# Kernel optimization log

Hardware: AMD Instinct MI355X
Metric: run time of the kernel (lower is better)

The kernel has to match this reference:

```python
import jax, jax.numpy as jnp
import numpy as np

N_NODES = 100000
N_REL = 3
HID = 256
LN_EPS = 1e-5
DENOM_EPS = 1e-8


def setup_inputs() -> dict:
    key = jax.random.key(0)
    ks = jax.random.split(key, 8)
    E = 300000
    return {
        "feat_text": jax.random.normal(ks[0], (N_NODES, 384), dtype=jnp.float32),
        "feat_image": jax.random.normal(ks[1], (N_NODES, 512), dtype=jnp.float32),
        "W_text": jax.random.normal(ks[2], (384, HID), dtype=jnp.float32) * 0.05,
        "W_image": jax.random.normal(ks[3], (512, HID), dtype=jnp.float32) * 0.05,
        "W_rel": jax.random.normal(ks[4], (N_REL, HID, HID), dtype=jnp.float32) * 0.05,
        "ln_gamma": jnp.ones((HID,), dtype=jnp.float32),
        "ln_beta": jnp.zeros((HID,), dtype=jnp.float32),
        "edge_weight": jax.random.uniform(ks[5], (E,), dtype=jnp.float32),
        "edge_index": jax.random.randint(ks[6], (2, E), 0, N_NODES),
        "edge_type": jax.random.randint(ks[7], (E,), 0, N_REL),
    }


def _layer_norm(x, gamma, beta):
    mu = jnp.mean(x, axis=-1, keepdims=True)
    var = jnp.mean(jnp.square(x - mu), axis=-1, keepdims=True)
    return (x - mu) * jax.lax.rsqrt(var + LN_EPS) * gamma + beta


def reference(feat_text, feat_image, W_text, W_image, W_rel, ln_gamma, ln_beta,
              edge_weight, edge_index, edge_type):
    # base embedding: mean of per-modality projections (fuse_mode='avg'), node 0 zeroed
    h0 = 0.5 * (feat_text @ W_text + feat_image @ W_image)  # [N, H]
    h0 = h0.at[0].set(0.0)

    src = edge_index[0]
    dst = edge_index[1]
    h_src = h0[src]  # [E, H] gather once, reused per relation

    aggregated = jnp.zeros_like(h0)
    for rel in range(N_REL):  # small fixed relation count
        w = jnp.where(edge_type == rel, edge_weight, 0.0)          # [E]
        msgs = (h_src @ W_rel[rel]) * w[:, None]                    # [E, H]
        agg_rel = jax.ops.segment_sum(msgs, dst, num_segments=N_NODES)   # [N, H]
        denom = jax.ops.segment_sum(w, dst, num_segments=N_NODES)        # [N]
        aggregated = aggregated + agg_rel / jnp.maximum(denom, DENOM_EPS)[:, None]

    # dropout=0.0 (identity)
    h1 = _layer_norm(h0 + aggregated, ln_gamma, ln_beta)
    h1 = h1.at[0].set(0.0)
    return h1
```

## Files before the change

kernel.cpp:

```cpp
#include <hip/hip_runtime.h>
#include <hip/hip_bf16.h>

#define HID 256
#define LN_EPS 1e-5f
#define DENOM_EPS 1e-8f

typedef __attribute__((ext_vector_type(8))) short short8;
typedef __attribute__((ext_vector_type(4))) float f32x4;

#define WP1_ELEMS (28 * 256 * 32)
#define WP2_ELEMS (24 * 256 * 32)

__device__ inline unsigned bfpk(float x, float y) {
    __hip_bfloat162 h = __float22bfloat162_rn(make_float2(x, y));
    return *reinterpret_cast<unsigned*>(&h);
}

__device__ inline void gld16(const void* g, void* l) {
    __builtin_amdgcn_global_load_lds(
        (const __attribute__((address_space(1))) void*)g,
        (__attribute__((address_space(3))) void*)l, 16, 0, 0);
}

__global__ __launch_bounds__(256) void kpack(
    const float* __restrict__ wt, const float* __restrict__ wi,
    const float* __restrict__ wrel,
    __hip_bfloat16* __restrict__ wp1, __hip_bfloat16* __restrict__ wp2)
{
    int idx = blockIdx.x * 256 + threadIdx.x;
    if (idx < WP1_ELEMS) {
        int kk = idx & 31, col = (idx >> 5) & 255, ks = idx >> 13;
        int k = ks * 32 + kk;
        float v = (k < 384) ? wt[k * 256 + col] : wi[(k - 384) * 256 + col];
        wp1[idx] = __float2bfloat16(v * 0.5f);
    } else {
        int j = idx - WP1_ELEMS;
        if (j < WP2_ELEMS) {
            int kk = j & 31, col = (j >> 5) & 255, ks = j >> 13;
            int k = ks * 32 + kk;
            wp2[j] = __float2bfloat16(wrel[k * 256 + col]);
        }
    }
}

__global__ __launch_bounds__(256) void kchain(
    const int* __restrict__ edst, int* __restrict__ head, int* __restrict__ nxt, int E)
{
    int e = blockIdx.x * 256 + threadIdx.x;
    if (e < E) nxt[e] = atomicExch(&head[edst[e]], e);
}

__global__ __launch_bounds__(256) void k2_gather(
    const float* __restrict__ h0, const int* __restrict__ esrc,
    const int* __restrict__ etype, const float* __restrict__ ew,
    const int* __restrict__ head, const int* __restrict__ nxt,
    __hip_bfloat16* __restrict__ S, int N)
{
    int gid = blockIdx.x * 256 + threadIdx.x;
    int d = gid >> 6;
    int lane = gid & 63;
    if (d >= N) return;

    f32x4 a0 = {0.f, 0.f, 0.f, 0.f}, a1 = a0, a2 = a0;
    float d0 = 0.f, d1 = 0.f, d2 = 0.f;

    int e = head[d];
    while (e >= 0) {
        int src = esrc[e];
        int ty = etype[e];
        float w = ew[e];
        const float4 h = *(const float4*)(h0 + (size_t)src * HID + lane * 4);
        f32x4 hw = {w * h.x, w * h.y, w * h.z, w * h.w};
        if (ty == 0)      { a0 += hw; d0 += w; }
        else if (ty == 1) { a1 += hw; d1 += w; }
        else              { a2 += hw; d2 += w; }
        e = nxt[e];
    }

    float i0 = 1.0f / fmaxf(d0, DENOM_EPS);
    float i1 = 1.0f / fmaxf(d1, DENOM_EPS);
    float i2 = 1.0f / fmaxf(d2, DENOM_EPS);
    __hip_bfloat16* row = S + (size_t)d * 768;
    uint2 p;
    p = make_uint2(bfpk(a0[0] * i0, a0[1] * i0), bfpk(a0[2] * i0, a0[3] * i0));
    *(uint2*)(row + 0   + lane * 4) = p;
    p = make_uint2(bfpk(a1[0] * i1, a1[1] * i1), bfpk(a1[2] * i1, a1[3] * i1));
    *(uint2*)(row + 256 + lane * 4) = p;
    p = make_uint2(bfpk(a2[0] * i2, a2[1] * i2), bfpk(a2[2] * i2, a2[3] * i2));
    *(uint2*)(row + 512 + lane * 4) = p;
}

template<int MODE>
__global__ __launch_bounds__(256, 4) void kgemm(
    const float* __restrict__ a0, const float* __restrict__ a1,
    const __hip_bfloat16* __restrict__ Sb,
    const __hip_bfloat16* __restrict__ wp,
    const float* h0in, const float* __restrict__ gamma,
    const float* __restrict__ beta, float* out, int N)
{
    constexpr int NSTEPS = MODE ? 24 : 28;
    constexpr int TB = MODE ? 4096 : 8192;
    __shared__ __align__(16) unsigned char As[3][TB];
    __shared__ float redS[MODE ? 64 : 1][4];
    __shared__ float redQ[MODE ? 64 : 1][4];

    const int t = threadIdx.x;
    const int lane = t & 63;
    const int w = t >> 6;
    const int m0 = blockIdx.x * 64;
    const int g = lane >> 4;

    auto stageA = [&](int ks, int buf) {
        if constexpr (MODE == 0) {
#pragma unroll
            for (int j = 0; j < 2; ++j) {
                int slot = j * 4 + w;
                int r = slot * 8 + (lane >> 3);
                int grow = m0 + r; if (grow >= N) grow = m0;
                int q = (lane & 7) ^ (lane >> 3);
                const float* src = (ks < 12)
                    ? (a0 + (size_t)grow * 384 + ks * 32 + q * 4)
                    : (a1 + (size_t)grow * 512 + (ks - 12) * 32 + q * 4);
                gld16(src, As[buf] + slot * 1024);
            }
        } else {
            int r = w * 16 + (lane >> 2);
            int grow = m0 + r; if (grow >= N) grow = m0;
            int q = (lane & 3) ^ ((lane >> 3) & 3);
            const __hip_bfloat16* src = Sb + (size_t)grow * 768 + ks * 32 + q * 8;
            gld16(src, As[buf] + w * 1024);
        }
    };

    f32x4 acc[4][4];
#pragma unroll
    for (int i = 0; i < 4; ++i)
#pragma unroll
        for (int j = 0; j < 4; ++j) acc[i][j] = (f32x4){0.f, 0.f, 0.f, 0.f};

    stageA(0, 0);

    for (int ks = 0; ks < NSTEPS; ++ks) {
        if (ks + 1 < NSTEPS) stageA(ks + 1, (ks + 1) % 3);
        short8 bf[4];
#pragma unroll
        for (int fc = 0; fc < 4; ++fc)
            bf[fc] = *(const short8*)((const short*)wp +
                      (size_t)(ks * 256 + w * 64 + fc * 16 + (lane & 15)) * 32 + g * 8);

        __syncthreads();

        const unsigned char* Ab = As[ks % 3];
        short8 af[4];
#pragma unroll
        for (int fr = 0; fr < 4; ++fr) {
            int r = fr * 16 + (lane & 15);
            if constexpr (MODE == 0) {
                const unsigned char* base = Ab + r * 128;
                f32x4 lo = *(const f32x4*)(base + ((2 * g) ^ (r & 7)) * 16);
                f32x4 hi = *(const f32x4*)(base + ((2 * g + 1) ^ (r & 7)) * 16);
                union { short8 s; unsigned u[4]; } cv;
                cv.u[0] = bfpk(lo[0], lo[1]);
                cv.u[1] = bfpk(lo[2], lo[3]);
                cv.u[2] = bfpk(hi[0], hi[1]);
                cv.u[3] = bfpk(hi[2], hi[3]);
                af[fr] = cv.s;
            } else {
                af[fr] = *(const short8*)(Ab + r * 64 + (g ^ ((r >> 1) & 3)) * 16);
            }
        }
#pragma unroll
        for (int fr = 0; fr < 4; ++fr)
#pragma unroll
            for (int fc = 0; fc < 4; ++fc)
                acc[fr][fc] = __builtin_amdgcn_mfma_f32_16x16x32_bf16(af[fr], bf[fc], acc[fr][fc], 0, 0, 0);
    }

    const int cbase = w * 64;

    if constexpr (MODE == 0) {
#pragma unroll
        for (int fr = 0; fr < 4; ++fr)
#pragma unroll
            for (int reg = 0; reg < 4; ++reg) {
                int grow = m0 + fr * 16 + g * 4 + reg;
                if (grow >= N) continue;
#pragma unroll
                for (int fc = 0; fc < 4; ++fc) {
                    float vv = acc[fr][fc][reg];
                    if (grow == 0) vv = 0.f;
                    out[(size_t)grow * 256 + cbase + fc * 16 + (lane & 15)] = vv;
                }
            }
    } else {
#pragma unroll
        for (int fr = 0; fr < 4; ++fr)
#pragma unroll
            for (int reg = 0; reg < 4; ++reg) {
                int grow = m0 + fr * 16 + g * 4 + reg;
                if (grow < N) {
#pragma unroll
                    for (int fc = 0; fc < 4; ++fc)
                        acc[fr][fc][reg] += h0in[(size_t)grow * 256 + cbase + fc * 16 + (lane & 15)];
                }
            }
#pragma unroll
        for (int fr = 0; fr < 4; ++fr)
#pragma unroll
            for (int reg = 0; reg < 4; ++reg) {
                float s = 0.f, q = 0.f;
#pragma unroll
                for (int fc = 0; fc < 4; ++fc) {
                    float vv = acc[fr][fc][reg];
                    s += vv; q += vv * vv;
                }
#pragma unroll
                for (int off = 1; off < 16; off <<= 1) {
                    s += __shfl_xor(s, off, 64);
                    q += __shfl_xor(q, off, 64);
                }
                if ((lane & 15) == 0) {
                    int rl = fr * 16 + g * 4 + reg;
                    redS[rl][w] = s;
                    redQ[rl][w] = q;
                }
            }
        __syncthreads();
        float g4[4], b4[4];
#pragma unroll
        for (int fc = 0; fc < 4; ++fc) {
            g4[fc] = gamma[cbase + fc * 16 + (lane & 15)];
            b4[fc] = beta[cbase + fc * 16 + (lane & 15)];
        }
#pragma unroll
        for (int fr = 0; fr < 4; ++fr)
#pragma unroll
            for (int reg = 0; reg < 4; ++reg) {
                int rl = fr * 16 + g * 4 + reg;
                int grow = m0 + rl;
                if (grow >= N) continue;
                float s = redS[rl][0] + redS[rl][1] + redS[rl][2] + redS[rl][3];
                float q = redQ[rl][0] + redQ[rl][1] + redQ[rl][2] + redQ[rl][3];
                float mu  = s * (1.f / 256.f);
                float var = q * (1.f / 256.f) - mu * mu;
                float rstd = rsqrtf(var + LN_EPS);
#pragma unroll
                for (int fc = 0; fc < 4; ++fc) {
                    float vv = (acc[fr][fc][reg] - mu) * rstd * g4[fc] + b4[fc];
                    if (grow == 0) vv = 0.f;
                    out[(size_t)grow * 256 + cbase + fc * 16 + (lane & 15)] = vv;
                }
            }
    }
}

extern "C" void kernel_launch(void* const* d_in, const int* in_sizes, int n_in,
                              void* d_out, int out_size, void* d_ws, size_t ws_size,
                              hipStream_t stream) {
    const int N = in_sizes[0] / 384;
    const int E = in_sizes[7];
    const float* ft    = (const float*)d_in[0];
    const float* fi    = (const float*)d_in[1];
    const float* wt    = (const float*)d_in[2];
    const float* wi    = (const float*)d_in[3];
    const float* wrel  = (const float*)d_in[4];
    const float* gamma = (const float*)d_in[5];
    const float* beta  = (const float*)d_in[6];
    const float* ew    = (const float*)d_in[7];
    const int*   eidx  = (const int*)d_in[8];
    const int*   etype = (const int*)d_in[9];
    float* out = (float*)d_out;

    __hip_bfloat16* S = (__hip_bfloat16*)d_ws;
    int* head = (int*)((char*)d_ws + (size_t)N * 768 * 2);
    int* nxt  = head + N;
    __hip_bfloat16* wp1 = (__hip_bfloat16*)(nxt + E);
    __hip_bfloat16* wp2 = wp1 + WP1_ELEMS;

    hipMemsetAsync(head, 0xFF, (size_t)N * sizeof(int), stream);

    kpack<<<(WP1_ELEMS + WP2_ELEMS + 255) / 256, 256, 0, stream>>>(wt, wi, wrel, wp1, wp2);

    kchain<<<(E + 255) / 256, 256, 0, stream>>>(eidx + E, head, nxt, E);

    const int gblocks = (N + 63) / 64;
    kgemm<0><<<gblocks, 256, 0, stream>>>(ft, fi, nullptr, wp1, nullptr, nullptr, nullptr, out, N);

    const int wblocks = (N + 3) / 4;
    k2_gather<<<wblocks, 256, 0, stream>>>(out, eidx, etype, ew, head, nxt, S, N);

    kgemm<1><<<gblocks, 256, 0, stream>>>(nullptr, nullptr, S, wp2, out, gamma, beta, out, N);
}
```

Before: 337.7 us.

## Drop LDS staging in GEMMs; gather writes MFMA-fragment layout for direct loads

The gather kernel now writes the aggregated relation features in a pre-tiled, MFMA-fragment-ordered layout per 64-row block, so the second GEMM can load A fragments straight from global memory without LDS staging or barriers. The first GEMM is split into its own kernel that reads fp32 features directly from global with per-lane vector loads and converts them to bf16 in registers. Gather blocks grow to 512 threads (8 nodes per block). This removes LDS traffic and syncs, but gives up async prefetch and multi-buffering, so more global-load latency is exposed, and the direct fp32 loads in the first GEMM may be less coalesced.

```diff
diff --git a/kernel.cpp b/kernel.cpp
--- a/kernel.cpp
+++ b/kernel.cpp
@@ -14,12 +14,6 @@
 __device__ inline unsigned bfpk(float x, float y) {
     __hip_bfloat162 h = __float22bfloat162_rn(make_float2(x, y));
     return *reinterpret_cast<unsigned*>(&h);
-}
-
-__device__ inline void gld16(const void* g, void* l) {
-    __builtin_amdgcn_global_load_lds(
-        (const __attribute__((address_space(1))) void*)g,
-        (__attribute__((address_space(3))) void*)l, 16, 0, 0);
 }
 
 __global__ __launch_bounds__(256) void kpack(
@@ -50,15 +44,15 @@
     if (e < E) nxt[e] = atomicExch(&head[edst[e]], e);
 }
 
-__global__ __launch_bounds__(256) void k2_gather(
+__global__ __launch_bounds__(512) void k2_gather(
     const float* __restrict__ h0, const int* __restrict__ esrc,
     const int* __restrict__ etype, const float* __restrict__ ew,
     const int* __restrict__ head, const int* __restrict__ nxt,
-    __hip_bfloat16* __restrict__ S, int N)
-{
-    int gid = blockIdx.x * 256 + threadIdx.x;
-    int d = gid >> 6;
-    int lane = gid & 63;
+    __hip_bfloat16* __restrict__ Sf, int N)
+{
+    int w = threadIdx.x >> 6;
+    int lane = threadIdx.x & 63;
+    int d = blockIdx.x * 8 + w;
     if (d >= N) return;
 
     f32x4 a0 = {0.f, 0.f, 0.f, 0.f}, a1 = a0, a2 = a0;
@@ -68,69 +62,45 @@
     while (e >= 0) {
         int src = esrc[e];
         int ty = etype[e];
-        float w = ew[e];
+        float w_ = ew[e];
         const float4 h = *(const float4*)(h0 + (size_t)src * HID + lane * 4);
-        f32x4 hw = {w * h.x, w * h.y, w * h.z, w * h.w};
-        if (ty == 0)      { a0 += hw; d0 += w; }
-        else if (ty == 1) { a1 += hw; d1 += w; }
-        else              { a2 += hw; d2 += w; }
+        f32x4 hw = {w_ * h.x, w_ * h.y, w_ * h.z, w_ * h.w};
+        if (ty == 0)      { a0 += hw; d0 += w_; }
+        else if (ty == 1) { a1 += hw; d1 += w_; }
+        else              { a2 += hw; d2 += w_; }
         e = nxt[e];
     }
 
     float i0 = 1.0f / fmaxf(d0, DENOM_EPS);
     float i1 = 1.0f / fmaxf(d1, DENOM_EPS);
     float i2 = 1.0f / fmaxf(d2, DENOM_EPS);
-    __hip_bfloat16* row = S + (size_t)d * 768;
-    uint2 p;
-    p = make_uint2(bfpk(a0[0] * i0, a0[1] * i0), bfpk(a0[2] * i0, a0[3] * i0));
-    *(uint2*)(row + 0   + lane * 4) = p;
-    p = make_uint2(bfpk(a1[0] * i1, a1[1] * i1), bfpk(a1[2] * i1, a1[3] * i1));
-    *(uint2*)(row + 256 + lane * 4) = p;
-    p = make_uint2(bfpk(a2[0] * i2, a2[1] * i2), bfpk(a2[2] * i2, a2[3] * i2));
-    *(uint2*)(row + 512 + lane * 4) = p;
-}
-
-template<int MODE>
-__global__ __launch_bounds__(256, 4) void kgemm(
-    const float* __restrict__ a0, const float* __restrict__ a1,
-    const __hip_bfloat16* __restrict__ Sb,
+
+    const int rb = d >> 6, r = d & 63;
+    const int g = (lane & 7) >> 1;
+    const int e0 = (lane & 1) * 4;
+    __hip_bfloat16* base = Sf + (size_t)rb * (24 * 256 * 8);
+#pragma unroll
+    for (int rel = 0; rel < 3; ++rel) {
+        const f32x4& a = rel == 0 ? a0 : (rel == 1 ? a1 : a2);
+        const float iv = rel == 0 ? i0 : (rel == 1 ? i1 : i2);
+        int ks = rel * 8 + (lane >> 3);
+        size_t off = ((size_t)ks * 256 + g * 64 + r) * 8 + e0;
+        uint2 p = make_uint2(bfpk(a[0] * iv, a[1] * iv), bfpk(a[2] * iv, a[3] * iv));
+        *(uint2*)(base + off) = p;
+    }
+}
+
+__global__ __launch_bounds__(256, 3) void kg0(
+    const float* __restrict__ ft, const float* __restrict__ fi,
     const __hip_bfloat16* __restrict__ wp,
-    const float* h0in, const float* __restrict__ gamma,
-    const float* __restrict__ beta, float* out, int N)
-{
-    constexpr int NSTEPS = MODE ? 24 : 28;
-    constexpr int TB = MODE ? 4096 : 8192;
-    __shared__ __align__(16) unsigned char As[3][TB];
-    __shared__ float redS[MODE ? 64 : 1][4];
-    __shared__ float redQ[MODE ? 64 : 1][4];
-
+    float* __restrict__ out, int N)
+{
     const int t = threadIdx.x;
     const int lane = t & 63;
     const int w = t >> 6;
     const int m0 = blockIdx.x * 64;
     const int g = lane >> 4;
-
-    auto stageA = [&](int ks, int buf) {
-        if constexpr (MODE == 0) {
-#pragma unroll
-            for (int j = 0; j < 2; ++j) {
-                int slot = j * 4 + w;
-                int r = slot * 8 + (lane >> 3);
-                int grow = m0 + r; if (grow >= N) grow = m0;
-                int q = (lane & 7) ^ (lane >> 3);
-                const float* src = (ks < 12)
-                    ? (a0 + (size_t)grow * 384 + ks * 32 + q * 4)
-                    : (a1 + (size_t)grow * 512 + (ks - 12) * 32 + q * 4);
-                gld16(src, As[buf] + slot * 1024);
-            }
-        } else {
-            int r = w * 16 + (lane >> 2);
-            int grow = m0 + r; if (grow >= N) grow = m0;
-            int q = (lane & 3) ^ ((lane >> 3) & 3);
-            const __hip_bfloat16* src = Sb + (size_t)grow * 768 + ks * 32 + q * 8;
-            gld16(src, As[buf] + w * 1024);
-        }
-    };
+    const int rl = lane & 15;
 
     f32x4 acc[4][4];
 #pragma unroll
@@ -138,37 +108,103 @@
 #pragma unroll
         for (int j = 0; j < 4; ++j) acc[i][j] = (f32x4){0.f, 0.f, 0.f, 0.f};
 
-    stageA(0, 0);
-
-    for (int ks = 0; ks < NSTEPS; ++ks) {
-        if (ks + 1 < NSTEPS) stageA(ks + 1, (ks + 1) % 3);
-        short8 bf[4];
-#pragma unroll
-        for (int fc = 0; fc < 4; ++fc)
-            bf[fc] = *(const short8*)((const short*)wp +
-                      (size_t)(ks * 256 + w * 64 + fc * 16 + (lane & 15)) * 32 + g * 8);
-
-        __syncthreads();
-
-        const unsigned char* Ab = As[ks % 3];
-        short8 af[4];
+    const short* wpb = (const short*)wp + ((size_t)w * 64 + rl) * 32 + g * 8;
+
+#pragma unroll 1
+    for (int seg = 0; seg < 2; ++seg) {
+        const float* __restrict__ A = seg ? fi : ft;
+        const int K = seg ? 512 : 384;
+        const int ns = seg ? 16 : 12;
+        const int ksb = seg ? 12 : 0;
+        const float* rp[4];
 #pragma unroll
         for (int fr = 0; fr < 4; ++fr) {
-            int r = fr * 16 + (lane & 15);
-            if constexpr (MODE == 0) {
-                const unsigned char* base = Ab + r * 128;
-                f32x4 lo = *(const f32x4*)(base + ((2 * g) ^ (r & 7)) * 16);
-                f32x4 hi = *(const f32x4*)(base + ((2 * g + 1) ^ (r & 7)) * 16);
-                union { short8 s; unsigned u[4]; } cv;
+            int grow = m0 + fr * 16 + rl;
+            if (grow >= N) grow = m0;
+            rp[fr] = A + (size_t)grow * K + g * 8;
+        }
+#pragma unroll 1
+        for (int s = 0; s < ns; ++s) {
+            short8 af[4];
+#pragma unroll
+            for (int fr = 0; fr < 4; ++fr) {
+                const float* ap = rp[fr] + s * 32;
+                f32x4 lo = *(const f32x4*)ap;
+                f32x4 hi = *(const f32x4*)(ap + 4);
+                union { short8 s8; unsigned u[4]; } cv;
                 cv.u[0] = bfpk(lo[0], lo[1]);
                 cv.u[1] = bfpk(lo[2], lo[3]);
                 cv.u[2] = bfpk(hi[0], hi[1]);
                 cv.u[3] = bfpk(hi[2], hi[3]);
-                af[fr] = cv.s;
-            } else {
-                af[fr] = *(const short8*)(Ab + r * 64 + (g ^ ((r >> 1) & 3)) * 16);
-            }
-        }
+                af[fr] = cv.s8;
+            }
+            short8 bf[4];
+            const short* bp = wpb + (size_t)(ksb + s) * 256 * 32;
+#pragma unroll
+            for (int fc = 0; fc < 4; ++fc)
+                bf[fc] = *(const short8*)(bp + fc * 16 * 32);
+#pragma unroll
+            for (int fr = 0; fr < 4; ++fr)
+#pragma unroll
+                for (int fc = 0; fc < 4; ++fc)
+                    acc[fr][fc] = __builtin_amdgcn_mfma_f32_16x16x32_bf16(af[fr], bf[fc], acc[fr][fc], 0, 0, 0);
+        }
+    }
+
+    const int cbase = w * 64;
+#pragma unroll
+    for (int fr = 0; fr < 4; ++fr)
+#pragma unroll
+        for (int reg = 0; reg < 4; ++reg) {
+            int grow = m0 + fr * 16 + g * 4 + reg;
+            if (grow >= N) continue;
+#pragma unroll
+            for (int fc = 0; fc < 4; ++fc) {
+                float vv = acc[fr][fc][reg];
+                if (grow == 0) vv = 0.f;
+                out[(size_t)grow * 256 + cbase + fc * 16 + rl] = vv;
+            }
+        }
+}
+
+__global__ __launch_bounds__(256, 4) void kg1(
+    const __hip_bfloat16* __restrict__ Sf,
+    const __hip_bfloat16* __restrict__ wp,
+    const float* h0in, const float* __restrict__ gamma,
+    const float* __restrict__ beta, float* __restrict__ out, int N)
+{
+    __shared__ float redS[64][4];
+    __shared__ float redQ[64][4];
+
+    const int t = threadIdx.x;
+    const int lane = t & 63;
+    const int w = t >> 6;
+    const int rb = blockIdx.x;
+    const int m0 = rb * 64;
+    const int g = lane >> 4;
+    const int rl = lane & 15;
+
+    f32x4 acc[4][4];
+#pragma unroll
+    for (int i = 0; i < 4; ++i)
+#pragma unroll
+        for (int j = 0; j < 4; ++j) acc[i][j] = (f32x4){0.f, 0.f, 0.f, 0.f};
+
+    const short* Ab = (const short*)(Sf + (size_t)rb * (24 * 256 * 8)) + ((size_t)g * 64 + rl) * 8;
+    const short* wpb = (const short*)wp + ((size_t)w * 64 + rl) * 32 + g * 8;
+
+#pragma unroll 1
+    for (int ks = 0; ks < 24; ++ks) {
+        short8 af[4];
+        const short* ap = Ab + (size_t)ks * 256 * 8;
+#pragma unroll
+        for (int fr = 0; fr < 4; ++fr)
+            af[fr] = *(const short8*)(ap + fr * 16 * 8);
+        short8 bf[4];
+        const short* bp = wpb + (size_t)ks * 256 * 32;
+#pragma unroll
+        for (int fc = 0; fc < 4; ++fc)
+            bf[fc] = *(const short8*)(bp + fc * 16 * 32);
 #pragma unroll
         for (int fr = 0; fr < 4; ++fr)
 #pragma unroll
@@ -177,81 +213,64 @@
     }
 
     const int cbase = w * 64;
-
-    if constexpr (MODE == 0) {
-#pragma unroll
-        for (int fr = 0; fr < 4; ++fr)
-#pragma unroll
-            for (int reg = 0; reg < 4; ++reg) {
-                int grow = m0 + fr * 16 + g * 4 + reg;
-                if (grow >= N) continue;
-#pragma unroll
-                for (int fc = 0; fc < 4; ++fc) {
-                    float vv = acc[fr][fc][reg];
-                    if (grow == 0) vv = 0.f;
-                    out[(size_t)grow * 256 + cbase + fc * 16 + (lane & 15)] = vv;
-                }
-            }
-    } else {
-#pragma unroll
-        for (int fr = 0; fr < 4; ++fr)
-#pragma unroll
-            for (int reg = 0; reg < 4; ++reg) {
-                int grow = m0 + fr * 16 + g * 4 + reg;
-                if (grow < N) {
-#pragma unroll
-                    for (int fc = 0; fc < 4; ++fc)
-                        acc[fr][fc][reg] += h0in[(size_t)grow * 256 + cbase + fc * 16 + (lane & 15)];
-                }
-            }
-#pragma unroll
-        for (int fr = 0; fr < 4; ++fr)
-#pragma unroll
-            for (int reg = 0; reg < 4; ++reg) {
-                float s = 0.f, q = 0.f;
-#pragma unroll
-                for (int fc = 0; fc < 4; ++fc) {
-                    float vv = acc[fr][fc][reg];
-                    s += vv; q += vv * vv;
-                }
-#pragma unroll
-                for (int off = 1; off < 16; off <<= 1) {
-                    s += __shfl_xor(s, off, 64);
-                    q += __shfl_xor(q, off, 64);
-                }
-                if ((lane & 15) == 0) {
-                    int rl = fr * 16 + g * 4 + reg;
-                    redS[rl][w] = s;
-                    redQ[rl][w] = q;
-                }
-            }
-        __syncthreads();
-        float g4[4], b4[4];
-#pragma unroll
-        for (int fc = 0; fc < 4; ++fc) {
-            g4[fc] = gamma[cbase + fc * 16 + (lane & 15)];
-            b4[fc] = beta[cbase + fc * 16 + (lane & 15)];
-        }
-#pragma unroll
-        for (int fr = 0; fr < 4; ++fr)
-#pragma unroll
-            for (int reg = 0; reg < 4; ++reg) {
-                int rl = fr * 16 + g * 4 + reg;
-                int grow = m0 + rl;
-                if (grow >= N) continue;
-                float s = redS[rl][0] + redS[rl][1] + redS[rl][2] + redS[rl][3];
-                float q = redQ[rl][0] + redQ[rl][1] + redQ[rl][2] + redQ[rl][3];
-                float mu  = s * (1.f / 256.f);
-                float var = q * (1.f / 256.f) - mu * mu;
-                float rstd = rsqrtf(var + LN_EPS);
-#pragma unroll
-                for (int fc = 0; fc < 4; ++fc) {
-                    float vv = (acc[fr][fc][reg] - mu) * rstd * g4[fc] + b4[fc];
-                    if (grow == 0) vv = 0.f;
-                    out[(size_t)grow * 256 + cbase + fc * 16 + (lane & 15)] = vv;
-                }
-            }
-    }
+#pragma unroll
+    for (int fr = 0; fr < 4; ++fr)
+#pragma unroll
+        for (int reg = 0; reg < 4; ++reg) {
+            int grow = m0 + fr * 16 + g * 4 + reg;
+            if (grow < N) {
+#pragma unroll
+                for (int fc = 0; fc < 4; ++fc)
+                    acc[fr][fc][reg] += h0in[(size_t)grow * 256 + cbase + fc * 16 + rl];
+            }
+        }
+#pragma unroll
+    for (int fr = 0; fr < 4; ++fr)
+#pragma unroll
+        for (int reg = 0; reg < 4; ++reg) {
+            float s = 0.f, q = 0.f;
+#pragma unroll
+            for (int fc = 0; fc < 4; ++fc) {
+                float vv = acc[fr][fc][reg];
+                s += vv; q += vv * vv;
+            }
+#pragma unroll
+            for (int off = 1; off < 16; off <<= 1) {
+                s += __shfl_xor(s, off, 64);
+                q += __shfl_xor(q, off, 64);
+            }
+            if (rl == 0) {
+                int rlidx = fr * 16 + g * 4 + reg;
+                redS[rlidx][w] = s;
+                redQ[rlidx][w] = q;
+            }
+        }
+    __syncthreads();
+    float g4[4], b4[4];
+#pragma unroll
+    for (int fc = 0; fc < 4; ++fc) {
+        g4[fc] = gamma[cbase + fc * 16 + rl];
+        b4[fc] = beta[cbase + fc * 16 + rl];
+    }
+#pragma unroll
+    for (int fr = 0; fr < 4; ++fr)
+#pragma unroll
+        for (int reg = 0; reg < 4; ++reg) {
+            int rlidx = fr * 16 + g * 4 + reg;
+            int grow = m0 + rlidx;
+            if (grow >= N) continue;
+            float s = redS[rlidx][0] + redS[rlidx][1] + redS[rlidx][2] + redS[rlidx][3];
+            float q = redQ[rlidx][0] + redQ[rlidx][1] + redQ[rlidx][2] + redQ[rlidx][3];
+            float mu  = s * (1.f / 256.f);
+            float var = q * (1.f / 256.f) - mu * mu;
+            float rstd = rsqrtf(var + LN_EPS);
+#pragma unroll
+            for (int fc = 0; fc < 4; ++fc) {
+                float vv = (acc[fr][fc][reg] - mu) * rstd * g4[fc] + b4[fc];
+                if (grow == 0) vv = 0.f;
+                out[(size_t)grow * 256 + cbase + fc * 16 + rl] = vv;
+            }
+        }
 }
 
 extern "C" void kernel_launch(void* const* d_in, const int* in_sizes, int n_in,
@@ -271,8 +290,9 @@
     const int*   etype = (const int*)d_in[9];
     float* out = (float*)d_out;
 
-    __hip_bfloat16* S = (__hip_bfloat16*)d_ws;
-    int* head = (int*)((char*)d_ws + (size_t)N * 768 * 2);
+    const int NRB = (N + 63) / 64;
+    __hip_bfloat16* Sf = (__hip_bfloat16*)d_ws;
+    int* head = (int*)((char*)d_ws + (size_t)NRB * 24 * 256 * 8 * 2);
     int* nxt  = head + N;
     __hip_bfloat16* wp1 = (__hip_bfloat16*)(nxt + E);
     __hip_bfloat16* wp2 = wp1 + WP1_ELEMS;
@@ -283,11 +303,9 @@
 
     kchain<<<(E + 255) / 256, 256, 0, stream>>>(eidx + E, head, nxt, E);
 
-    const int gblocks = (N + 63) / 64;
-    kgemm<0><<<gblocks, 256, 0, stream>>>(ft, fi, nullptr, wp1, nullptr, nullptr, nullptr, out, N);
-
-    const int wblocks = (N + 3) / 4;
-    k2_gather<<<wblocks, 256, 0, stream>>>(out, eidx, etype, ew, head, nxt, S, N);
-
-    kgemm<1><<<gblocks, 256, 0, stream>>>(nullptr, nullptr, S, wp2, out, gamma, beta, out, N);
-}
+    kg0<<<NRB, 256, 0, stream>>>(ft, fi, wp1, out, N);
+
+    k2_gather<<<(N + 7) / 8, 512, 0, stream>>>(out, eidx, etype, ew, head, nxt, Sf, N);
+
+    kg1<<<NRB, 256, 0, stream>>>(Sf, wp2, out, gamma, beta, out, N);
+}
```

Result: slower. 583.9 us (+72.9%).

## Apply relation weights per node before aggregation and fuse gather with layernorm

Applied to the files above, without the earlier changes.

The order of operations is changed so the relation projections run on node embeddings (Y_r = h0 @ W_rel[r]) inside the first GEMM kernel, reusing the h0 tile held in LDS. The edge gather then reads bf16 Y rows, normalizes, adds h0 and applies layernorm in one kernel, removing the separate second GEMM and its fp32 h0 round trip. The first GEMM also gains an explicit double-buffered pipeline with manual waitcnt and barriers. In exchange it writes 3N×256 bf16 intermediates, and h0 is now stored in bf16, which lowers precision in the residual path.

```diff
diff --git a/kernel.cpp b/kernel.cpp
--- a/kernel.cpp
+++ b/kernel.cpp
@@ -20,6 +20,16 @@
     __builtin_amdgcn_global_load_lds(
         (const __attribute__((address_space(1))) void*)g,
         (__attribute__((address_space(3))) void*)l, 16, 0, 0);
+}
+
+__device__ inline f32x4 bf4_to_f32(uint2 p) {
+    union { float f; unsigned u; } c;
+    f32x4 r;
+    c.u = (p.x & 0xFFFFu) << 16;  r[0] = c.f;
+    c.u = (p.x & 0xFFFF0000u);    r[1] = c.f;
+    c.u = (p.y & 0xFFFFu) << 16;  r[2] = c.f;
+    c.u = (p.y & 0xFFFF0000u);    r[3] = c.f;
+    return r;
 }
 
 __global__ __launch_bounds__(256) void kpack(
@@ -50,87 +60,40 @@
     if (e < E) nxt[e] = atomicExch(&head[edst[e]], e);
 }
 
-__global__ __launch_bounds__(256) void k2_gather(
-    const float* __restrict__ h0, const int* __restrict__ esrc,
-    const int* __restrict__ etype, const float* __restrict__ ew,
-    const int* __restrict__ head, const int* __restrict__ nxt,
-    __hip_bfloat16* __restrict__ S, int N)
+__global__ __launch_bounds__(256, 3) void kg0f(
+    const float* __restrict__ ft, const float* __restrict__ fi,
+    const __hip_bfloat16* __restrict__ wp1,
+    const __hip_bfloat16* __restrict__ wp2,
+    __hip_bfloat16* __restrict__ h0b,
+    __hip_bfloat16* __restrict__ Yb, int N)
 {
-    int gid = blockIdx.x * 256 + threadIdx.x;
-    int d = gid >> 6;
-    int lane = gid & 63;
-    if (d >= N) return;
-
-    f32x4 a0 = {0.f, 0.f, 0.f, 0.f}, a1 = a0, a2 = a0;
-    float d0 = 0.f, d1 = 0.f, d2 = 0.f;
-
-    int e = head[d];
-    while (e >= 0) {
-        int src = esrc[e];
-        int ty = etype[e];
-        float w = ew[e];
-        const float4 h = *(const float4*)(h0 + (size_t)src * HID + lane * 4);
-        f32x4 hw = {w * h.x, w * h.y, w * h.z, w * h.w};
-        if (ty == 0)      { a0 += hw; d0 += w; }
-        else if (ty == 1) { a1 += hw; d1 += w; }
-        else              { a2 += hw; d2 += w; }
-        e = nxt[e];
-    }
-
-    float i0 = 1.0f / fmaxf(d0, DENOM_EPS);
-    float i1 = 1.0f / fmaxf(d1, DENOM_EPS);
-    float i2 = 1.0f / fmaxf(d2, DENOM_EPS);
-    __hip_bfloat16* row = S + (size_t)d * 768;
-    uint2 p;
-    p = make_uint2(bfpk(a0[0] * i0, a0[1] * i0), bfpk(a0[2] * i0, a0[3] * i0));
-    *(uint2*)(row + 0   + lane * 4) = p;
-    p = make_uint2(bfpk(a1[0] * i1, a1[1] * i1), bfpk(a1[2] * i1, a1[3] * i1));
-    *(uint2*)(row + 256 + lane * 4) = p;
-    p = make_uint2(bfpk(a2[0] * i2, a2[1] * i2), bfpk(a2[2] * i2, a2[3] * i2));
-    *(uint2*)(row + 512 + lane * 4) = p;
-}
-
-template<int MODE>
-__global__ __launch_bounds__(256, 4) void kgemm(
-    const float* __restrict__ a0, const float* __restrict__ a1,
-    const __hip_bfloat16* __restrict__ Sb,
-    const __hip_bfloat16* __restrict__ wp,
-    const float* h0in, const float* __restrict__ gamma,
-    const float* __restrict__ beta, float* out, int N)
-{
-    constexpr int NSTEPS = MODE ? 24 : 28;
-    constexpr int TB = MODE ? 4096 : 8192;
-    __shared__ __align__(16) unsigned char As[3][TB];
-    __shared__ float redS[MODE ? 64 : 1][4];
-    __shared__ float redQ[MODE ? 64 : 1][4];
-
+    __shared__ __align__(16) unsigned char lds[32768];
     const int t = threadIdx.x;
     const int lane = t & 63;
     const int w = t >> 6;
     const int m0 = blockIdx.x * 64;
     const int g = lane >> 4;
+    const int rl = lane & 15;
 
     auto stageA = [&](int ks, int buf) {
-        if constexpr (MODE == 0) {
-#pragma unroll
-            for (int j = 0; j < 2; ++j) {
-                int slot = j * 4 + w;
-                int r = slot * 8 + (lane >> 3);
-                int grow = m0 + r; if (grow >= N) grow = m0;
-                int q = (lane & 7) ^ (lane >> 3);
-                const float* src = (ks < 12)
-                    ? (a0 + (size_t)grow * 384 + ks * 32 + q * 4)
-                    : (a1 + (size_t)grow * 512 + (ks - 12) * 32 + q * 4);
-                gld16(src, As[buf] + slot * 1024);
-            }
-        } else {
-            int r = w * 16 + (lane >> 2);
+#pragma unroll
+        for (int j = 0; j < 2; ++j) {
+            int slot = j * 4 + w;
+            int r = slot * 8 + (lane >> 3);
             int grow = m0 + r; if (grow >= N) grow = m0;
-            int q = (lane & 3) ^ ((lane >> 3) & 3);
-            const __hip_bfloat16* src = Sb + (size_t)grow * 768 + ks * 32 + q * 8;
-            gld16(src, As[buf] + w * 1024);
+            int q = (lane & 7) ^ (lane >> 3);
+            const float* src = (ks < 12)
+                ? (ft + (size_t)grow * 384 + ks * 32 + q * 4)
+                : (fi + (size_t)grow * 512 + (ks - 12) * 32 + q * 4);
+            gld16(src, lds + buf * 8192 + slot * 1024);
         }
     };
+    auto loadB1 = [&](short8 (&bf)[4], int ks) {
+#pragma unroll
+        for (int fc = 0; fc < 4; ++fc)
+            bf[fc] = *(const short8*)((const short*)wp1 +
+                      (size_t)(ks * 256 + w * 64 + fc * 16 + rl) * 32 + g * 8);
+    };
 
     f32x4 acc[4][4];
 #pragma unroll
@@ -138,47 +101,112 @@
 #pragma unroll
         for (int j = 0; j < 4; ++j) acc[i][j] = (f32x4){0.f, 0.f, 0.f, 0.f};
 
-    stageA(0, 0);
-
-    for (int ks = 0; ks < NSTEPS; ++ks) {
-        if (ks + 1 < NSTEPS) stageA(ks + 1, (ks + 1) % 3);
-        short8 bf[4];
-#pragma unroll
-        for (int fc = 0; fc < 4; ++fc)
-            bf[fc] = *(const short8*)((const short*)wp +
-                      (size_t)(ks * 256 + w * 64 + fc * 16 + (lane & 15)) * 32 + g * 8);
-
-        __syncthreads();
-
-        const unsigned char* Ab = As[ks % 3];
+    auto compute1 = [&](int ks, short8 (&bf)[4]) {
+        const unsigned char* Ab = lds + (ks % 3) * 8192;
         short8 af[4];
 #pragma unroll
         for (int fr = 0; fr < 4; ++fr) {
-            int r = fr * 16 + (lane & 15);
-            if constexpr (MODE == 0) {
-                const unsigned char* base = Ab + r * 128;
-                f32x4 lo = *(const f32x4*)(base + ((2 * g) ^ (r & 7)) * 16);
-                f32x4 hi = *(const f32x4*)(base + ((2 * g + 1) ^ (r & 7)) * 16);
-                union { short8 s; unsigned u[4]; } cv;
-                cv.u[0] = bfpk(lo[0], lo[1]);
-                cv.u[1] = bfpk(lo[2], lo[3]);
-                cv.u[2] = bfpk(hi[0], hi[1]);
-                cv.u[3] = bfpk(hi[2], hi[3]);
-                af[fr] = cv.s;
-            } else {
-                af[fr] = *(const short8*)(Ab + r * 64 + (g ^ ((r >> 1) & 3)) * 16);
-            }
+            int r = fr * 16 + rl;
+            const unsigned char* base = Ab + r * 128;
+            f32x4 lo = *(const f32x4*)(base + ((2 * g) ^ (r & 7)) * 16);
+            f32x4 hi = *(const f32x4*)(base + ((2 * g + 1) ^ (r & 7)) * 16);
+            union { short8 s8; unsigned u[4]; } cv;
+            cv.u[0] = bfpk(lo[0], lo[1]);
+            cv.u[1] = bfpk(lo[2], lo[3]);
+            cv.u[2] = bfpk(hi[0], hi[1]);
+            cv.u[3] = bfpk(hi[2], hi[3]);
+            af[fr] = cv.s8;
         }
 #pragma unroll
         for (int fr = 0; fr < 4; ++fr)
 #pragma unroll
             for (int fc = 0; fc < 4; ++fc)
                 acc[fr][fc] = __builtin_amdgcn_mfma_f32_16x16x32_bf16(af[fr], bf[fc], acc[fr][fc], 0, 0, 0);
-    }
+    };
+
+    short8 bfe[4], bfo[4];
+    stageA(0, 0);
+    stageA(1, 1);
+    loadB1(bfe, 0);
+
+#pragma unroll 1
+    for (int p = 0; p < 14; ++p) {
+        const int ks = 2 * p;
+        asm volatile("s_waitcnt vmcnt(6)" ::: "memory");
+        __builtin_amdgcn_s_barrier();
+        __builtin_amdgcn_sched_barrier(0);
+        if (ks + 2 < 28) stageA(ks + 2, (ks + 2) % 3);
+        loadB1(bfo, ks + 1);
+        compute1(ks, bfe);
+        if (p == 13) asm volatile("s_waitcnt vmcnt(0)" ::: "memory");
+        else         asm volatile("s_waitcnt vmcnt(6)" ::: "memory");
+        __builtin_amdgcn_s_barrier();
+        __builtin_amdgcn_sched_barrier(0);
+        if (ks + 3 < 28) stageA(ks + 3, (ks + 3) % 3);
+        if (ks + 2 < 28) loadB1(bfe, ks + 2);
+        compute1(ks + 1, bfo);
+    }
+    __syncthreads();
 
     const int cbase = w * 64;
-
-    if constexpr (MODE == 0) {
+#pragma unroll
+    for (int fr = 0; fr < 4; ++fr)
+#pragma unroll
+        for (int reg = 0; reg < 4; ++reg) {
+            int rloc = fr * 16 + g * 4 + reg;
+            int grow = m0 + rloc;
+#pragma unroll
+            for (int fc = 0; fc < 4; ++fc) {
+                float vv = acc[fr][fc][reg];
+                if (grow == 0) vv = 0.f;
+                int col = cbase + fc * 16 + rl;
+                int phys = (col >> 3) ^ (rloc & 31);
+                *(__hip_bfloat16*)(lds + rloc * 512 + phys * 16 + (col & 7) * 2) =
+                    __float2bfloat16(vv);
+            }
+        }
+    __syncthreads();
+
+#pragma unroll
+    for (int j = 0; j < 8; ++j) {
+        int ci = t + j * 256;
+        int r = ci >> 5, c = ci & 31;
+        int grow = m0 + r;
+        if (grow < N) {
+            short8 v = *(const short8*)(lds + r * 512 + ((c ^ (r & 31)) * 16));
+            *(short8*)(h0b + (size_t)grow * 256 + c * 8) = v;
+        }
+    }
+
+#pragma unroll 1
+    for (int rel = 0; rel < 3; ++rel) {
+        f32x4 acc2[4][4];
+#pragma unroll
+        for (int i = 0; i < 4; ++i)
+#pragma unroll
+            for (int j = 0; j < 4; ++j) acc2[i][j] = (f32x4){0.f, 0.f, 0.f, 0.f};
+
+#pragma unroll
+        for (int ks = 0; ks < 8; ++ks) {
+            short8 af[4];
+#pragma unroll
+            for (int fr = 0; fr < 4; ++fr) {
+                int r = fr * 16 + rl;
+                int phys = (ks * 4 + g) ^ (r & 31);
+                af[fr] = *(const short8*)(lds + r * 512 + phys * 16);
+            }
+            short8 bf[4];
+#pragma unroll
+            for (int fc = 0; fc < 4; ++fc)
+                bf[fc] = *(const short8*)((const short*)wp2 +
+                          (size_t)((rel * 8 + ks) * 256 + w * 64 + fc * 16 + rl) * 32 + g * 8);
+#pragma unroll
+            for (int fr = 0; fr < 4; ++fr)
+#pragma unroll
+                for (int fc = 0; fc < 4; ++fc)
+                    acc2[fr][fc] = __builtin_amdgcn_mfma_f32_16x16x32_bf16(af[fr], bf[fc], acc2[fr][fc], 0, 0, 0);
+        }
+        __hip_bfloat16* Yr = Yb + (size_t)rel * N * 256;
 #pragma unroll
         for (int fr = 0; fr < 4; ++fr)
 #pragma unroll
@@ -186,72 +214,73 @@
                 int grow = m0 + fr * 16 + g * 4 + reg;
                 if (grow >= N) continue;
 #pragma unroll
-                for (int fc = 0; fc < 4; ++fc) {
-                    float vv = acc[fr][fc][reg];
-                    if (grow == 0) vv = 0.f;
-                    out[(size_t)grow * 256 + cbase + fc * 16 + (lane & 15)] = vv;
-                }
+                for (int fc = 0; fc < 4; ++fc)
+                    Yr[(size_t)grow * 256 + cbase + fc * 16 + rl] =
+                        __float2bfloat16(acc2[fr][fc][reg]);
             }
-    } else {
-#pragma unroll
-        for (int fr = 0; fr < 4; ++fr)
-#pragma unroll
-            for (int reg = 0; reg < 4; ++reg) {
-                int grow = m0 + fr * 16 + g * 4 + reg;
-                if (grow < N) {
-#pragma unroll
-                    for (int fc = 0; fc < 4; ++fc)
-                        acc[fr][fc][reg] += h0in[(size_t)grow * 256 + cbase + fc * 16 + (lane & 15)];
-                }
-            }
-#pragma unroll
-        for (int fr = 0; fr < 4; ++fr)
-#pragma unroll
-            for (int reg = 0; reg < 4; ++reg) {
-                float s = 0.f, q = 0.f;
-#pragma unroll
-                for (int fc = 0; fc < 4; ++fc) {
-                    float vv = acc[fr][fc][reg];
-                    s += vv; q += vv * vv;
-                }
-#pragma unroll
-                for (int off = 1; off < 16; off <<= 1) {
-                    s += __shfl_xor(s, off, 64);
-                    q += __shfl_xor(q, off, 64);
-                }
-                if ((lane & 15) == 0) {
-                    int rl = fr * 16 + g * 4 + reg;
-                    redS[rl][w] = s;
-                    redQ[rl][w] = q;
-                }
-            }
-        __syncthreads();
-        float g4[4], b4[4];
-#pragma unroll
-        for (int fc = 0; fc < 4; ++fc) {
-            g4[fc] = gamma[cbase + fc * 16 + (lane & 15)];
-            b4[fc] = beta[cbase + fc * 16 + (lane & 15)];
-        }
-#pragma unroll
-        for (int fr = 0; fr < 4; ++fr)
-#pragma unroll
-            for (int reg = 0; reg < 4; ++reg) {
-                int rl = fr * 16 + g * 4 + reg;
-                int grow = m0 + rl;
-                if (grow >= N) continue;
-                float s = redS[rl][0] + redS[rl][1] + redS[rl][2] + redS[rl][3];
-                float q = redQ[rl][0] + redQ[rl][1] + redQ[rl][2] + redQ[rl][3];
-                float mu  = s * (1.f / 256.f);
-                float var = q * (1.f / 256.f) - mu * mu;
-                float rstd = rsqrtf(var + LN_EPS);
-#pragma unroll
-                for (int fc = 0; fc < 4; ++fc) {
-                    float vv = (acc[fr][fc][reg] - mu) * rstd * g4[fc] + b4[fc];
-                    if (grow == 0) vv = 0.f;
-                    out[(size_t)grow * 256 + cbase + fc * 16 + (lane & 15)] = vv;
-                }
-            }
-    }
+    }
+}
+
+__global__ __launch_bounds__(512) void k2ln(
+    const __hip_bfloat16* __restrict__ Yb,
+    const __hip_bfloat16* __restrict__ h0b,
+    const int* __restrict__ esrc, const int* __restrict__ etype,
+    const float* __restrict__ ew,
+    const int* __restrict__ head, const int* __restrict__ nxt,
+    const float* __restrict__ gamma, const float* __restrict__ beta,
+    float* __restrict__ out, int N)
+{
+    int w = threadIdx.x >> 6;
+    int lane = threadIdx.x & 63;
+    int d = blockIdx.x * 8 + w;
+    if (d >= N) return;
+
+    f32x4 a0 = {0.f, 0.f, 0.f, 0.f}, a1 = a0, a2 = a0;
+    float d0 = 0.f, d1 = 0.f, d2 = 0.f;
+
+    int e = head[d];
+    while (e >= 0) {
+        int src = esrc[e];
+        int ty = etype[e];
+        float we = ew[e];
+        uint2 yv = *(const uint2*)(Yb + ((size_t)ty * N + src) * 256 + lane * 4);
+        f32x4 y = bf4_to_f32(yv);
+        if (ty == 0)      { a0 += we * y; d0 += we; }
+        else if (ty == 1) { a1 += we * y; d1 += we; }
+        else              { a2 += we * y; d2 += we; }
+        e = nxt[e];
+    }
+
+    float i0 = 1.0f / fmaxf(d0, DENOM_EPS);
+    float i1 = 1.0f / fmaxf(d1, DENOM_EPS);
+    float i2 = 1.0f / fmaxf(d2, DENOM_EPS);
+
+    f32x4 h = bf4_to_f32(*(const uint2*)(h0b + (size_t)d * 256 + lane * 4));
+    f32x4 x;
+#pragma unroll
+    for (int j = 0; j < 4; ++j)
+        x[j] = h[j] + a0[j] * i0 + a1[j] * i1 + a2[j] * i2;
+
+    float s = x[0] + x[1] + x[2] + x[3];
+    float q = x[0] * x[0] + x[1] * x[1] + x[2] * x[2] + x[3] * x[3];
+#pragma unroll
+    for (int off = 1; off < 64; off <<= 1) {
+        s += __shfl_xor(s, off, 64);
+        q += __shfl_xor(q, off, 64);
+    }
+    float mu  = s * (1.f / 256.f);
+    float var = q * (1.f / 256.f) - mu * mu;
+    float rstd = rsqrtf(var + LN_EPS);
+
+    const float4 g4 = *(const float4*)(gamma + lane * 4);
+    const float4 b4 = *(const float4*)(beta + lane * 4);
+    float4 o;
+    o.x = (x[0] - mu) * rstd * g4.x + b4.x;
+    o.y = (x[1] - mu) * rstd * g4.y + b4.y;
+    o.z = (x[2] - mu) * rstd * g4.z + b4.z;
+    o.w = (x[3] - mu) * rstd * g4.w + b4.w;
+    if (d == 0) o = make_float4(0.f, 0.f, 0.f, 0.f);
+    *(float4*)(out + (size_t)d * 256 + lane * 4) = o;
 }
 
 extern "C" void kernel_launch(void* const* d_in, const int* in_sizes, int n_in,
@@ -271,8 +300,9 @@
     const int*   etype = (const int*)d_in[9];
     float* out = (float*)d_out;
 
-    __hip_bfloat16* S = (__hip_bfloat16*)d_ws;
-    int* head = (int*)((char*)d_ws + (size_t)N * 768 * 2);
+    __hip_bfloat16* Yb  = (__hip_bfloat16*)d_ws;
+    __hip_bfloat16* h0b = Yb + (size_t)3 * N * 256;
+    int* head = (int*)(h0b + (size_t)N * 256);
     int* nxt  = head + N;
     __hip_bfloat16* wp1 = (__hip_bfloat16*)(nxt + E);
     __hip_bfloat16* wp2 = wp1 + WP1_ELEMS;
@@ -284,10 +314,8 @@
     kchain<<<(E + 255) / 256, 256, 0, stream>>>(eidx + E, head, nxt, E);
 
     const int gblocks = (N + 63) / 64;
-    kgemm<0><<<gblocks, 256, 0, stream>>>(ft, fi, nullptr, wp1, nullptr, nullptr, nullptr, out, N);
-
-    const int wblocks = (N + 3) / 4;
-    k2_gather<<<wblocks, 256, 0, stream>>>(out, eidx, etype, ew, head, nxt, S, N);
-
-    kgemm<1><<<gblocks, 256, 0, stream>>>(nullptr, nullptr, S, wp2, out, gamma, beta, out, N);
-}
+    kg0f<<<gblocks, 256, 0, stream>>>(ft, fi, wp1, wp2, h0b, Yb, N);
+
+    k2ln<<<(N + 7) / 8, 512, 0, stream>>>(Yb, h0b, eidx, etype, ew, head, nxt,
+                                          gamma, beta, out, N);
+}
```

New measurement: 410.1 us. 1.21x slower.
